# Kernel tuning notes

Hardware: AMD Instinct MI355X
Metric: run time of the kernel (lower is better)

## Reference

```python
import jax, jax.numpy as jnp
import numpy as np

B, S, IN, OUT, L, R = 2, 8192, 2048, 2048, 4, 32


def setup_inputs() -> dict:
    key = jax.random.key(0)
    ks = jax.random.split(key, 6)
    return {
        "x": jax.random.normal(ks[0], (B, S, IN), dtype=jnp.float32),
        "weight": jax.random.normal(ks[1], (OUT, IN), dtype=jnp.float32) * 0.02,
        "bias": jax.random.normal(ks[2], (OUT,), dtype=jnp.float32) * 0.02,
        "downs": jax.random.normal(ks[3], (L, R, IN), dtype=jnp.float32) * 0.02,
        "ups": jax.random.normal(ks[4], (L, OUT, R), dtype=jnp.float32) * 0.02,
        "scales": jax.random.uniform(ks[5], (L,), dtype=jnp.float32),
    }


def reference(x, weight, bias, downs, ups, scales):
    # Base linear: y = x @ W.T + b
    y = jnp.einsum("bsi,oi->bso", x, weight) + bias
    # Low-rank LoRA deltas, grouped across adapters:
    # tmp[b,s,l,r] = x @ down_l.T ; delta = sum_l scale_l * tmp_l @ up_l.T
    tmp = jnp.einsum("bsi,lri->bslr", x, downs)  # [B,S,L,R]
    tmp = tmp * scales[None, None, :, None]       # fold per-adapter scale
    delta = jnp.einsum("bslr,lor->bso", tmp, ups)  # [B,S,OUT]
    return y + delta
```

## Files before the change

kernel.cpp:

```cpp
#include <hip/hip_runtime.h>

#define M_DIM 16384
#define N_DIM 2048
#define K_DIM 2048
#define L_AD 4
#define R_AD 32

typedef __bf16 bf16_t;
typedef bf16_t bf16x8 __attribute__((ext_vector_type(8)));
typedef bf16_t bf16x4 __attribute__((ext_vector_type(4)));
typedef float f32x4 __attribute__((ext_vector_type(4)));
typedef float f32x16 __attribute__((ext_vector_type(16)));

#define BM 128
#define BN 128
#define BK 64

__device__ __forceinline__ void async_load16(const void* g, void* l) {
  __builtin_amdgcn_global_load_lds(
      (const __attribute__((address_space(1))) unsigned int*)g,
      (__attribute__((address_space(3))) unsigned int*)l, 16, 0, 0);
}

__global__ __launch_bounds__(256) void convert_x_kernel(
    const float* __restrict__ X, bf16_t* __restrict__ Xb) {
  const size_t base = ((size_t)blockIdx.x * 256 + threadIdx.x) * 8;
  f32x4 lo = *(const f32x4*)(X + base);
  f32x4 hi = *(const f32x4*)(X + base + 4);
  bf16x8 v;
  v[0] = (bf16_t)lo[0]; v[1] = (bf16_t)lo[1];
  v[2] = (bf16_t)lo[2]; v[3] = (bf16_t)lo[3];
  v[4] = (bf16_t)hi[0]; v[5] = (bf16_t)hi[1];
  v[6] = (bf16_t)hi[2]; v[7] = (bf16_t)hi[3];
  *(bf16x8*)(Xb + base) = v;
}

__global__ __launch_bounds__(256) void build_weff_kernel(
    const float* __restrict__ W, const float* __restrict__ downs,
    const float* __restrict__ ups, const float* __restrict__ scales,
    bf16_t* __restrict__ weff) {
  __shared__ float up_s[64 * 129];
  __shared__ float down_s[128 * 64];
  const int t = threadIdx.x;
  const int n0 = blockIdx.y * 64;
  const int k0 = blockIdx.x * 64;

  for (int l = 0; l < L_AD; ++l) {
    const float sc = scales[l];
    const float* up_l = ups + (size_t)l * N_DIM * R_AD;
    #pragma unroll
    for (int j = 0; j < 8; ++j) {
      int flat = j * 256 + t;
      int nl = flat >> 5, r = flat & 31;
      up_s[nl * 129 + l * 32 + r] = sc * up_l[(size_t)(n0 + nl) * R_AD + r];
    }
  }
  #pragma unroll
  for (int j = 0; j < 32; ++j) {
    int flat = j * 256 + t;
    int lr = flat >> 6, kk = flat & 63;
    down_s[lr * 64 + kk] = downs[(size_t)lr * K_DIM + k0 + kk];
  }
  __syncthreads();

  const int tn = t >> 4, tk = t & 15;
  float acc[4][4] = {};
  for (int lr = 0; lr < L_AD * R_AD; ++lr) {
    f32x4 b = *(const f32x4*)&down_s[lr * 64 + tk * 4];
    #pragma unroll
    for (int u = 0; u < 4; ++u) {
      float a = up_s[(tn * 4 + u) * 129 + lr];
      #pragma unroll
      for (int v = 0; v < 4; ++v) acc[u][v] += a * b[v];
    }
  }
  #pragma unroll
  for (int u = 0; u < 4; ++u) {
    int n = n0 + tn * 4 + u;
    f32x4 wv = *(const f32x4*)&W[(size_t)n * K_DIM + k0 + tk * 4];
    bf16x4 o;
    #pragma unroll
    for (int v = 0; v < 4; ++v) o[v] = (bf16_t)(acc[u][v] + wv[v]);
    *(bf16x4*)&weff[(size_t)n * K_DIM + k0 + tk * 4] = o;
  }
}

__global__ __launch_bounds__(256) void gemm_bf16_kernel(
    const bf16_t* __restrict__ Xb, const bf16_t* __restrict__ Wb,
    const float* __restrict__ bias, float* __restrict__ out) {
  __shared__ __align__(16) bf16_t As[BM * BK];
  __shared__ __align__(16) bf16_t Bs[BN * BK];

  const int t = threadIdx.x;
  const int lane = t & 63;
  const int wv = t >> 6;
  const int wm = wv >> 1, wn = wv & 1;
  const int l5 = lane & 31;
  const int half = lane >> 5;
  const int m0 = blockIdx.y * BM;
  const int n0 = blockIdx.x * BN;

  const int srow = t >> 3;
  const int soct = t & 7;

  f32x16 acc[2][2] = {};

  float bn[2];
  #pragma unroll
  for (int j = 0; j < 2; ++j) bn[j] = bias[n0 + wn * 64 + j * 32 + l5];

  for (int kt = 0; kt < K_DIM / BK; ++kt) {
    const int kg = kt * BK;
    #pragma unroll
    for (int j = 0; j < 4; ++j) {
      int row = j * 32 + srow;
      int c = soct ^ (row & 7);
      async_load16(Wb + (size_t)(n0 + row) * K_DIM + kg + c * 8,
                   &Bs[(size_t)(row * 8 + soct) * 8]);
      async_load16(Xb + (size_t)(m0 + row) * K_DIM + kg + c * 8,
                   &As[(size_t)(row * 8 + soct) * 8]);
    }
    __syncthreads();

    #pragma unroll
    for (int ks = 0; ks < 4; ++ks) {
      bf16x8 af[2], bfr[2];
      #pragma unroll
      for (int i = 0; i < 2; ++i) {
        int row = wm * 64 + i * 32 + l5;
        int p = (ks * 2 + half) ^ (row & 7);
        af[i] = *(const bf16x8*)&As[row * BK + p * 8];
      }
      #pragma unroll
      for (int j = 0; j < 2; ++j) {
        int row = wn * 64 + j * 32 + l5;
        int p = (ks * 2 + half) ^ (row & 7);
        bfr[j] = *(const bf16x8*)&Bs[row * BK + p * 8];
      }
      #pragma unroll
      for (int i = 0; i < 2; ++i) {
        #pragma unroll
        for (int j = 0; j < 2; ++j)
          acc[i][j] = __builtin_amdgcn_mfma_f32_32x32x16_bf16(af[i], bfr[j], acc[i][j], 0, 0, 0);
      }
    }
    __syncthreads();
  }

  #pragma unroll
  for (int i = 0; i < 2; ++i) {
    #pragma unroll
    for (int j = 0; j < 2; ++j) {
      int n = n0 + wn * 64 + j * 32 + l5;
      #pragma unroll
      for (int r = 0; r < 16; ++r) {
        int m = m0 + wm * 64 + i * 32 + (r & 3) + 8 * (r >> 2) + 4 * half;
        out[(size_t)m * N_DIM + n] = acc[i][j][r] + bn[j];
      }
    }
  }
}

#define SA 72
__global__ __launch_bounds__(256) void lora_gemm_fallback(
    const float* __restrict__ X, const bf16_t* __restrict__ Wb,
    const float* __restrict__ bias, float* __restrict__ out) {
  __shared__ __align__(16) bf16_t As[BM * SA];
  __shared__ __align__(16) bf16_t Bs[BN * BK];

  const int t = threadIdx.x;
  const int lane = t & 63;
  const int wv = t >> 6;
  const int wm = wv >> 1, wn = wv & 1;
  const int col = lane & 15, quad = lane >> 4;
  const int m0 = blockIdx.y * BM;
  const int n0 = blockIdx.x * BN;
  const int srow = t >> 3;
  const int soct = t & 7;

  f32x4 acc[4][4] = {};
  float bn[4];
  #pragma unroll
  for (int j = 0; j < 4; ++j) bn[j] = bias[n0 + wn * 64 + j * 16 + col];

  for (int kt = 0; kt < K_DIM / BK; ++kt) {
    const int kg = kt * BK;
    #pragma unroll
    for (int j = 0; j < 4; ++j) {
      int n = j * 32 + srow;
      int c = soct ^ (n & 7);
      async_load16(Wb + (size_t)(n0 + n) * K_DIM + kg + c * 8,
                   &Bs[(size_t)(j * 256 + t) * 8]);
    }
    #pragma unroll
    for (int j = 0; j < 4; ++j) {
      int m = j * 32 + srow;
      const f32x4* src = (const f32x4*)(X + (size_t)(m0 + m) * K_DIM + kg + soct * 8);
      f32x4 lo = src[0], hi = src[1];
      bf16x8 v;
      v[0] = (bf16_t)lo[0]; v[1] = (bf16_t)lo[1];
      v[2] = (bf16_t)lo[2]; v[3] = (bf16_t)lo[3];
      v[4] = (bf16_t)hi[0]; v[5] = (bf16_t)hi[1];
      v[6] = (bf16_t)hi[2]; v[7] = (bf16_t)hi[3];
      *(bf16x8*)&As[m * SA + soct * 8] = v;
    }
    __syncthreads();

    #pragma unroll
    for (int ks = 0; ks < 2; ++ks) {
      bf16x8 af[4], bfr[4];
      #pragma unroll
      for (int i = 0; i < 4; ++i)
        af[i] = *(const bf16x8*)&As[(wm * 64 + i * 16 + col) * SA + ks * 32 + quad * 8];
      #pragma unroll
      for (int j = 0; j < 4; ++j) {
        int n = wn * 64 + j * 16 + col;
        int p = (ks * 4 + quad) ^ (n & 7);
        bfr[j] = *(const bf16x8*)&Bs[n * BK + p * 8];
      }
      #pragma unroll
      for (int i = 0; i < 4; ++i) {
        #pragma unroll
        for (int j = 0; j < 4; ++j)
          acc[i][j] = __builtin_amdgcn_mfma_f32_16x16x32_bf16(af[i], bfr[j], acc[i][j], 0, 0, 0);
      }
    }
    __syncthreads();
  }

  #pragma unroll
  for (int i = 0; i < 4; ++i) {
    #pragma unroll
    for (int r = 0; r < 4; ++r) {
      int m = m0 + wm * 64 + i * 16 + quad * 4 + r;
      float* orow = out + (size_t)m * N_DIM + n0 + wn * 64 + col;
      #pragma unroll
      for (int j = 0; j < 4; ++j)
        orow[j * 16] = acc[i][j][r] + bn[j];
    }
  }
}

extern "C" void kernel_launch(void* const* d_in, const int* in_sizes, int n_in,
                              void* d_out, int out_size, void* d_ws, size_t ws_size,
                              hipStream_t stream) {
  const float* x      = (const float*)d_in[0];
  const float* weight = (const float*)d_in[1];
  const float* bias   = (const float*)d_in[2];
  const float* downs  = (const float*)d_in[3];
  const float* ups    = (const float*)d_in[4];
  const float* scales = (const float*)d_in[5];
  float* out = (float*)d_out;

  const size_t weff_bytes = (size_t)N_DIM * K_DIM * 2;
  const size_t xb_bytes   = (size_t)M_DIM * K_DIM * 2;
  bf16_t* weff = (bf16_t*)d_ws;

  dim3 g1(K_DIM / 64, N_DIM / 64);
  build_weff_kernel<<<g1, 256, 0, stream>>>(weight, downs, ups, scales, weff);

  dim3 g2(N_DIM / BN, M_DIM / BM);
  if (ws_size >= weff_bytes + xb_bytes) {
    bf16_t* xb = (bf16_t*)((char*)d_ws + weff_bytes);
    const size_t n_elem = (size_t)M_DIM * K_DIM;
    convert_x_kernel<<<(unsigned)(n_elem / (256 * 8)), 256, 0, stream>>>(x, xb);
    gemm_bf16_kernel<<<g2, 256, 0, stream>>>(xb, weff, bias, out);
  } else {
    lora_gemm_fallback<<<g2, 256, 0, stream>>>(x, weff, bias, out);
  }
}
```

Before: 393.0 us.

## Replace bf16 GEMM with 256x256 double-buffered, ping-pong scheduled 8-wave kernel

Swaps the 128x128 single-buffered bf16 GEMM for a 256x256-tile kernel with 512 threads. It double-buffers LDS, interleaves async global-to-LDS loads with MFMA clusters under explicit barriers, vmcnt waits and setprio, and swizzles block order for L2 reuse. The goal is to hide memory latency and raise MFMA utilization on the dominant GEMM. In exchange it uses 128 KB of LDS per block and many accumulator registers, and the hand-written waitcnt and barrier schedule is fragile.

```diff
diff --git a/kernel.cpp b/kernel.cpp
--- a/kernel.cpp
+++ b/kernel.cpp
@@ -10,7 +10,6 @@
 typedef bf16_t bf16x8 __attribute__((ext_vector_type(8)));
 typedef bf16_t bf16x4 __attribute__((ext_vector_type(4)));
 typedef float f32x4 __attribute__((ext_vector_type(4)));
-typedef float f32x16 __attribute__((ext_vector_type(16)));
 
 #define BM 128
 #define BN 128
@@ -85,80 +84,156 @@
   }
 }
 
-__global__ __launch_bounds__(256) void gemm_bf16_kernel(
+#define BARRIER() __builtin_amdgcn_s_barrier()
+#define LGKM0() asm volatile("s_waitcnt lgkmcnt(0)" ::: "memory")
+#define VMCNT6() asm volatile("s_waitcnt vmcnt(6)" ::: "memory")
+
+__global__ __launch_bounds__(512, 2) void gemm_bf16_256(
     const bf16_t* __restrict__ Xb, const bf16_t* __restrict__ Wb,
     const float* __restrict__ bias, float* __restrict__ out) {
-  __shared__ __align__(16) bf16_t As[BM * BK];
-  __shared__ __align__(16) bf16_t Bs[BN * BK];
+  __shared__ __align__(16) bf16_t sm[2][2][16384];
+
+  const int orig = blockIdx.x;
+  const int swz = (orig & 7) * 64 + (orig >> 3);
+  const int m0 = (swz >> 3) * 256;
+  const int n0 = (swz & 7) * 256;
 
   const int t = threadIdx.x;
-  const int lane = t & 63;
-  const int wv = t >> 6;
-  const int wm = wv >> 1, wn = wv & 1;
-  const int l5 = lane & 31;
-  const int half = lane >> 5;
-  const int m0 = blockIdx.y * BM;
-  const int n0 = blockIdx.x * BN;
-
-  const int srow = t >> 3;
-  const int soct = t & 7;
-
-  f32x16 acc[2][2] = {};
-
-  float bn[2];
-  #pragma unroll
-  for (int j = 0; j < 2; ++j) bn[j] = bias[n0 + wn * 64 + j * 32 + l5];
-
-  for (int kt = 0; kt < K_DIM / BK; ++kt) {
-    const int kg = kt * BK;
-    #pragma unroll
-    for (int j = 0; j < 4; ++j) {
-      int row = j * 32 + srow;
-      int c = soct ^ (row & 7);
-      async_load16(Wb + (size_t)(n0 + row) * K_DIM + kg + c * 8,
-                   &Bs[(size_t)(row * 8 + soct) * 8]);
-      async_load16(Xb + (size_t)(m0 + row) * K_DIM + kg + c * 8,
-                   &As[(size_t)(row * 8 + soct) * 8]);
-    }
-    __syncthreads();
-
-    #pragma unroll
-    for (int ks = 0; ks < 4; ++ks) {
-      bf16x8 af[2], bfr[2];
-      #pragma unroll
-      for (int i = 0; i < 2; ++i) {
-        int row = wm * 64 + i * 32 + l5;
-        int p = (ks * 2 + half) ^ (row & 7);
-        af[i] = *(const bf16x8*)&As[row * BK + p * 8];
-      }
-      #pragma unroll
-      for (int j = 0; j < 2; ++j) {
-        int row = wn * 64 + j * 32 + l5;
-        int p = (ks * 2 + half) ^ (row & 7);
-        bfr[j] = *(const bf16x8*)&Bs[row * BK + p * 8];
-      }
-      #pragma unroll
-      for (int i = 0; i < 2; ++i) {
-        #pragma unroll
-        for (int j = 0; j < 2; ++j)
-          acc[i][j] = __builtin_amdgcn_mfma_f32_32x32x16_bf16(af[i], bfr[j], acc[i][j], 0, 0, 0);
-      }
-    }
-    __syncthreads();
-  }
-
-  #pragma unroll
-  for (int i = 0; i < 2; ++i) {
-    #pragma unroll
-    for (int j = 0; j < 2; ++j) {
-      int n = n0 + wn * 64 + j * 32 + l5;
-      #pragma unroll
-      for (int r = 0; r < 16; ++r) {
-        int m = m0 + wm * 64 + i * 32 + (r & 3) + 8 * (r >> 2) + 4 * half;
-        out[(size_t)m * N_DIM + n] = acc[i][j][r] + bn[j];
-      }
-    }
-  }
+  const int l = t & 63;
+  const int w = t >> 6;
+  const int wm = w >> 2, wn = w & 3;
+  const int col = l & 15, quad = l >> 4;
+
+  const int d0 = w * 64 + l;
+  const int row0 = d0 >> 3;
+  const int c0 = (d0 & 7) ^ (row0 & 7);
+  const bf16_t* Ab = Xb + (size_t)(m0 + row0) * K_DIM + c0 * 8;
+  const bf16_t* Bb = Wb + (size_t)(n0 + row0) * K_DIM + c0 * 8;
+
+  const int arow = wm * 128 + col;
+  const int brow = wn * 64 + col;
+
+  float bn[4];
+  #pragma unroll
+  for (int g = 0; g < 4; ++g) bn[g] = bias[n0 + wn * 64 + g * 16 + col];
+
+  f32x4 acc[8][4] = {};
+  bf16x8 aA[4][2], bB[4][2];
+
+#define STG(Gb, B_, OP, H, KT)                                                 \
+  do {                                                                         \
+    async_load16((Gb) + ((size_t)(H)*128) * K_DIM + (size_t)(KT)*64,           \
+                 &sm[B_][OP][(H)*8192 + d0 * 8]);                              \
+    async_load16((Gb) + ((size_t)(H)*128 + 64) * K_DIM + (size_t)(KT)*64,      \
+                 &sm[B_][OP][(H)*8192 + (d0 + 512) * 8]);                      \
+  } while (0)
+
+#define LDA(F0, B_)                                                            \
+  do {                                                                         \
+    _Pragma("unroll") for (int f_ = 0; f_ < 4; ++f_) {                         \
+      const int R_ = arow + ((F0) + f_) * 16;                                  \
+      const int rl_ = R_ & 127, h_ = R_ >> 7;                                  \
+      _Pragma("unroll") for (int ks_ = 0; ks_ < 2; ++ks_) {                    \
+        const int sl_ = (ks_ * 4 + quad) ^ (rl_ & 7);                          \
+        aA[f_][ks_] =                                                          \
+            *(const bf16x8*)&sm[B_][0][h_ * 8192 + (rl_ * 8 + sl_) * 8];       \
+      }                                                                        \
+    }                                                                          \
+  } while (0)
+
+#define LDB(B_)                                                                \
+  do {                                                                         \
+    _Pragma("unroll") for (int g_ = 0; g_ < 4; ++g_) {                         \
+      const int R_ = brow + g_ * 16;                                           \
+      const int rl_ = R_ & 127, h_ = R_ >> 7;                                  \
+      _Pragma("unroll") for (int ks_ = 0; ks_ < 2; ++ks_) {                    \
+        const int sl_ = (ks_ * 4 + quad) ^ (rl_ & 7);                          \
+        bB[g_][ks_] =                                                          \
+            *(const bf16x8*)&sm[B_][1][h_ * 8192 + (rl_ * 8 + sl_) * 8];       \
+      }                                                                        \
+    }                                                                          \
+  } while (0)
+
+#define MF(FA, G0)                                                             \
+  do {                                                                         \
+    __builtin_amdgcn_s_setprio(1);                                             \
+    _Pragma("unroll") for (int f_ = 0; f_ < 4; ++f_)                           \
+        _Pragma("unroll") for (int g_ = 0; g_ < 2; ++g_)                       \
+            _Pragma("unroll") for (int ks_ = 0; ks_ < 2; ++ks_)                \
+                acc[(FA) + f_][(G0) + g_] =                                    \
+                    __builtin_amdgcn_mfma_f32_16x16x32_bf16(                   \
+                        aA[f_][ks_], bB[(G0) + g_][ks_],                       \
+                        acc[(FA) + f_][(G0) + g_], 0, 0, 0);                   \
+    __builtin_amdgcn_s_setprio(0);                                             \
+  } while (0)
+
+  STG(Bb, 0, 1, 0, 0); STG(Bb, 0, 1, 1, 0);
+  STG(Ab, 0, 0, 0, 0); STG(Ab, 0, 0, 1, 0);
+  STG(Bb, 1, 1, 0, 1); STG(Bb, 1, 1, 1, 1);
+  STG(Ab, 1, 0, 0, 1);
+  VMCNT6();
+  BARRIER();
+
+  for (int j = 0; j < 16; ++j) {
+    const int k1 = 2 * j + 1;
+    const int kt2 = (2 * j + 2 < 32) ? 2 * j + 2 : 31;
+    const int kt3 = (2 * j + 3 < 32) ? 2 * j + 3 : 31;
+
+    LDA(0, 0); LDB(0);
+    STG(Ab, 1, 0, 1, k1);
+    BARRIER(); LGKM0();
+    MF(0, 0);
+    BARRIER();
+    STG(Bb, 0, 1, 0, kt2);
+    BARRIER(); LGKM0();
+    MF(0, 2);
+    BARRIER();
+    LDA(4, 0);
+    STG(Bb, 0, 1, 1, kt2);
+    BARRIER(); LGKM0();
+    MF(4, 2);
+    BARRIER();
+    STG(Ab, 0, 0, 0, kt2);
+    BARRIER(); LGKM0();
+    MF(4, 0);
+    VMCNT6();
+    BARRIER();
+    LDA(0, 1); LDB(1);
+    STG(Ab, 0, 0, 1, kt2);
+    BARRIER(); LGKM0();
+    MF(0, 0);
+    BARRIER();
+    STG(Bb, 1, 1, 0, kt3);
+    BARRIER(); LGKM0();
+    MF(0, 2);
+    BARRIER();
+    LDA(4, 1);
+    STG(Bb, 1, 1, 1, kt3);
+    BARRIER(); LGKM0();
+    MF(4, 2);
+    BARRIER();
+    STG(Ab, 1, 0, 0, kt3);
+    BARRIER(); LGKM0();
+    MF(4, 0);
+    VMCNT6();
+    BARRIER();
+  }
+
+  #pragma unroll
+  for (int f = 0; f < 8; ++f) {
+    const int m = m0 + wm * 128 + f * 16 + quad * 4;
+    #pragma unroll
+    for (int g = 0; g < 4; ++g) {
+      const int n = n0 + wn * 64 + g * 16 + col;
+      float* op = out + (size_t)m * N_DIM + n;
+      #pragma unroll
+      for (int r = 0; r < 4; ++r) op[(size_t)r * N_DIM] = acc[f][g][r] + bn[g];
+    }
+  }
+#undef STG
+#undef LDA
+#undef LDB
+#undef MF
 }
 
 #define SA 72
@@ -259,13 +334,14 @@
   dim3 g1(K_DIM / 64, N_DIM / 64);
   build_weff_kernel<<<g1, 256, 0, stream>>>(weight, downs, ups, scales, weff);
 
-  dim3 g2(N_DIM / BN, M_DIM / BM);
   if (ws_size >= weff_bytes + xb_bytes) {
     bf16_t* xb = (bf16_t*)((char*)d_ws + weff_bytes);
     const size_t n_elem = (size_t)M_DIM * K_DIM;
     convert_x_kernel<<<(unsigned)(n_elem / (256 * 8)), 256, 0, stream>>>(x, xb);
-    gemm_bf16_kernel<<<g2, 256, 0, stream>>>(xb, weff, bias, out);
+    gemm_bf16_256<<<dim3((M_DIM / 256) * (N_DIM / 256)), 512, 0, stream>>>(
+        xb, weff, bias, out);
   } else {
+    dim3 g2(N_DIM / BN, M_DIM / BM);
     lora_gemm_fallback<<<g2, 256, 0, stream>>>(x, weff, bias, out);
   }
 }
```

Result: faster. 376.7 us (-4.1%).
